# Kernel tuning notes

Hardware: AMD Instinct MI355X
Metric: run time of the kernel (lower is better)

Reference implementation:

```python
import jax, jax.numpy as jnp
import numpy as np

H = 2048      # hidden_size
K = 1024      # bottleneck_size
R = 3         # number of roles
B = 8         # batch
S = 2048      # sequence length
LN_EPS = 1e-5


def setup_inputs() -> dict:
    key = jax.random.key(0)
    ks = jax.random.split(key, 8)
    # torch nn.Linear default init ~ U(-1/sqrt(fan_in), 1/sqrt(fan_in)); scale similarly
    sd_d = 1.0 / np.sqrt(H)
    sd_u = 1.0 / np.sqrt(K)
    return {
        "role": jax.random.randint(ks[0], (B,), 0, R),
        "hidden_states": jax.random.normal(ks[1], (B, S, H), dtype=jnp.float32),
        # stacked per-role adapter params
        "W_down": jax.random.uniform(ks[2], (R, H, K), jnp.float32, -sd_d, sd_d),
        "b_down": jax.random.uniform(ks[3], (R, K), jnp.float32, -sd_d, sd_d),
        "W_up": jax.random.uniform(ks[4], (R, K, H), jnp.float32, -sd_u, sd_u),
        "b_up": jax.random.uniform(ks[5], (R, H), jnp.float32, -sd_u, sd_u),
        "gamma": jnp.ones((R, H), jnp.float32),
        "beta": jnp.zeros((R, H), jnp.float32),
    }


def reference(role, hidden_states, W_down, b_down, W_up, b_up, gamma, beta):
    # gather per-sample adapter params by role id: [B, H, K] etc.
    h = jnp.einsum("bsh,bhk->bsk", hidden_states, W_down[role]) + b_down[role][:, None, :]
    h = jax.nn.gelu(h, approximate=False)  # torch nn.GELU default = exact erf
    u = jnp.einsum("bsk,bkh->bsh", h, W_up[role]) + b_up[role][:, None, :]
    y = hidden_states + u
    # LayerNorm over last dim
    mean = jnp.mean(y, axis=-1, keepdims=True)
    var = jnp.mean(jnp.square(y - mean), axis=-1, keepdims=True)
    yn = (y - mean) * jax.lax.rsqrt(var + LN_EPS)
    return yn * gamma[role][:, None, :] + beta[role][:, None, :]
```

## Files before the change

kernel.cpp:

```cpp
#include <hip/hip_runtime.h>
#include <hip/hip_bf16.h>

#define H 2048
#define K 1024
#define R 3
#define BB 8
#define S 2048

typedef __bf16 bf16x8 __attribute__((ext_vector_type(8)));
typedef float f32x4 __attribute__((ext_vector_type(4)));
typedef unsigned short ushort8 __attribute__((ext_vector_type(8)));

static __device__ __forceinline__ unsigned short f2bf(float f) {
    unsigned int u = __float_as_uint(f);
    u += 0x7FFFu + ((u >> 16) & 1u);
    return (unsigned short)(u >> 16);
}

#define GLOAD_LDS16(g, l)                                                      \
    __builtin_amdgcn_global_load_lds(                                          \
        (const __attribute__((address_space(1))) void*)(g),                    \
        (__attribute__((address_space(3))) void*)(l), 16, 0, 0)

__global__ __launch_bounds__(256) void cvt_hs(const float* __restrict__ in,
                                              unsigned short* __restrict__ out,
                                              int n8) {
    int stride = gridDim.x * blockDim.x;
    for (int i = blockIdx.x * blockDim.x + threadIdx.x; i < n8; i += stride) {
        const float4* p = (const float4*)(in + (size_t)i * 8);
        float4 a = p[0], b = p[1];
        union { unsigned short us[8]; ushort8 v; } o;
        o.us[0] = f2bf(a.x); o.us[1] = f2bf(a.y);
        o.us[2] = f2bf(a.z); o.us[3] = f2bf(a.w);
        o.us[4] = f2bf(b.x); o.us[5] = f2bf(b.y);
        o.us[6] = f2bf(b.z); o.us[7] = f2bf(b.w);
        *(ushort8*)(out + (size_t)i * 8) = o.v;
    }
}

__global__ __launch_bounds__(256) void tpose(const float* __restrict__ in,
                                             unsigned short* __restrict__ out,
                                             int rows, int cols) {
    __shared__ float tile[32][33];
    int rr = blockIdx.z;
    const float* ip = in + (size_t)rr * rows * cols;
    unsigned short* op = out + (size_t)rr * rows * cols;
    int x = blockIdx.x * 32 + threadIdx.x;
    int y0 = blockIdx.y * 32 + threadIdx.y;
#pragma unroll
    for (int j = 0; j < 32; j += 8)
        tile[threadIdx.y + j][threadIdx.x] = ip[(size_t)(y0 + j) * cols + x];
    __syncthreads();
    int ox = blockIdx.y * 32 + threadIdx.x;
    int oy0 = blockIdx.x * 32 + threadIdx.y;
#pragma unroll
    for (int j = 0; j < 32; j += 8)
        op[(size_t)(oy0 + j) * rows + ox] = f2bf(tile[threadIdx.x][threadIdx.y + j]);
}

template <int KC, int EPI>
__global__ __launch_bounds__(512, 4) void gemm_tlp(
    const unsigned short* __restrict__ A, const unsigned short* __restrict__ Bt,
    const int* __restrict__ role, const float* __restrict__ bias,
    const unsigned short* __restrict__ resid, void* __restrict__ Out,
    float2* __restrict__ Part, int N) {
    constexpr int NT = KC / 32;
    __shared__ char smem[73728];
    const int tid = threadIdx.x;
    const int wid = tid >> 6, lane = tid & 63;
    const int wm = wid >> 2, wn = wid & 3;
    const int lr = lane & 15, lc = lane >> 4;

    const int nx = N >> 8;
    const int cpx = gridDim.x >> 3;
    const int orig = (blockIdx.x & 7) * cpx + (blockIdx.x >> 3);
    const int tn = orig % nx;
    const int tmz = orig / nx;
    const int tm = tmz & 15;
    const int z = tmz >> 4;
    const int r = role[z];

    const char* Ab = (const char*)(A + ((size_t)z * S + (size_t)tm * 128) * KC);
    const char* Bb = (const char*)(Bt + ((size_t)r * N + (size_t)tn * 256) * KC);

    const int P16 = tid * 16;
    const int srowA = P16 >> 6;
    const int sslot = ((P16 >> 4) & 3) ^ ((srowA >> 1) & 3);
    const size_t sgA = (size_t)srowA * (KC * 2) + sslot * 16;

#define STGA(sb, kt) GLOAD_LDS16(Ab + sgA + (kt) * 64, smem + (sb) + P16)
#define STGB(sb, kt, c)                                                        \
    GLOAD_LDS16(Bb + (size_t)((c) * 128 + srowA) * (KC * 2) + sslot * 16 +     \
                    (kt) * 64,                                                 \
                smem + (sb) + 8192 + (c) * 8192 + P16)
#define STAGE3(sb, kt) do { STGA(sb, kt); STGB(sb, kt, 0); STGB(sb, kt, 1); } while (0)

    STAGE3(0, 0);
    STAGE3(24576, 1);
    asm volatile("s_waitcnt vmcnt(3)" ::: "memory");
    __builtin_amdgcn_s_barrier();

    f32x4 acc[4][4] = {};
    const int ck = (lc ^ ((lr >> 1) & 3)) << 4;
    const char* sm = smem;

    int sA = 0, sB = 24576, sC = 49152;
#pragma unroll 1
    for (int t = 0; t < NT; ++t) {
        const bool pf = (t + 2) < NT;
        if (pf) STAGE3(sC, t + 2);
        bf16x8 a[4], b[4];
#pragma unroll
        for (int i = 0; i < 4; i++)
            a[i] = *(const bf16x8*)(sm + sA + ((wm * 64 + i * 16 + lr) << 6) + ck);
#pragma unroll
        for (int j = 0; j < 4; j++)
            b[j] = *(const bf16x8*)(sm + sA + 8192 + ((wn * 64 + j * 16 + lr) << 6) + ck);
        __builtin_amdgcn_s_setprio(1);
#pragma unroll
        for (int i = 0; i < 4; i++)
#pragma unroll
            for (int j = 0; j < 4; j++)
                acc[i][j] = __builtin_amdgcn_mfma_f32_16x16x32_bf16(a[i], b[j], acc[i][j], 0, 0, 0);
        __builtin_amdgcn_s_setprio(0);
        if (t < NT - 1) {
            if (pf) asm volatile("s_waitcnt vmcnt(3)" ::: "memory");
            else    asm volatile("s_waitcnt vmcnt(0)" ::: "memory");
            __builtin_amdgcn_s_barrier();
        }
        int tmp = sA; sA = sB; sB = sC; sC = tmp;
    }
#undef STGA
#undef STGB
#undef STAGE3

    const int base_m = tm * 128 + wm * 64;
    const int base_n = tn * 256 + wn * 64;
    float bn[4];
    const float* bp = bias + (size_t)r * N + base_n;
#pragma unroll
    for (int j = 0; j < 4; j++) bn[j] = bp[j * 16 + lr];

    if (EPI == 0) {
        unsigned short* o = (unsigned short*)Out;
#pragma unroll
        for (int i = 0; i < 4; i++) {
#pragma unroll
            for (int j = 0; j < 4; j++) {
#pragma unroll
                for (int q = 0; q < 4; q++) {
                    size_t grow = (size_t)z * S + base_m + i * 16 + lc * 4 + q;
                    int col = base_n + j * 16 + lr;
                    float x = acc[i][j][q] + bn[j];
                    float g = 0.5f * x * (1.0f + erff(x * 0.70710678118654752f));
                    o[grow * N + col] = f2bf(g);
                }
            }
        }
    } else {
        unsigned short* o = (unsigned short*)Out;
        float* pl = (float*)smem;
        __syncthreads();
#pragma unroll
        for (int i = 0; i < 4; i++) {
#pragma unroll
            for (int q = 0; q < 4; q++) {
                size_t grow = (size_t)z * S + base_m + i * 16 + lc * 4 + q;
                float s = 0.f, sq = 0.f;
#pragma unroll
                for (int j = 0; j < 4; j++) {
                    int col = base_n + j * 16 + lr;
                    float rv = __uint_as_float(((unsigned)resid[grow * (size_t)N + col]) << 16);
                    float y = acc[i][j][q] + bn[j] + rv;
                    o[grow * (size_t)N + col] = f2bf(y);
                    s += y; sq += y * y;
                }
#pragma unroll
                for (int off = 1; off < 16; off <<= 1) {
                    s  += __shfl_xor(s, off);
                    sq += __shfl_xor(sq, off);
                }
                if (lr == 0) {
                    int rloc = wm * 64 + i * 16 + lc * 4 + q;
                    pl[wn * 128 + rloc] = s;
                    pl[512 + wn * 128 + rloc] = sq;
                }
            }
        }
        __syncthreads();
        if (tid < 128) {
            float s  = pl[tid] + pl[128 + tid] + pl[256 + tid] + pl[384 + tid];
            float sq = pl[512 + tid] + pl[640 + tid] + pl[768 + tid] + pl[896 + tid];
            size_t grow = (size_t)z * S + tm * 128 + tid;
            Part[(size_t)tn * (BB * S) + grow] = make_float2(s, sq);
        }
    }
}

__global__ __launch_bounds__(256) void ln2(const unsigned short* __restrict__ ybf,
                                           const float2* __restrict__ part,
                                           const int* __restrict__ role,
                                           const float* __restrict__ gamma,
                                           const float* __restrict__ beta,
                                           float* __restrict__ out) {
    int row = blockIdx.x;
    int z = row >> 11;
    int r = role[z];
    float s = 0.f, ss = 0.f;
#pragma unroll
    for (int nb = 0; nb < 8; nb++) {
        float2 p = part[(size_t)nb * (BB * S) + row];
        s += p.x; ss += p.y;
    }
    float mean = s * (1.0f / H);
    float var = ss * (1.0f / H) - mean * mean;
    float rstd = rsqrtf(var + 1e-5f);
    int t = threadIdx.x;
    ushort8 yv = ((const ushort8*)(ybf + (size_t)row * H))[t];
    const float4* gp = (const float4*)(gamma + (size_t)r * H);
    const float4* bp = (const float4*)(beta + (size_t)r * H);
    float4 g0 = gp[2 * t], g1 = gp[2 * t + 1];
    float4 b0 = bp[2 * t], b1 = bp[2 * t + 1];
    float yo[8];
#pragma unroll
    for (int e = 0; e < 8; e++)
        yo[e] = (__uint_as_float(((unsigned)yv[e]) << 16) - mean) * rstd;
    float4 r0, r1;
    r0.x = yo[0] * g0.x + b0.x; r0.y = yo[1] * g0.y + b0.y;
    r0.z = yo[2] * g0.z + b0.z; r0.w = yo[3] * g0.w + b0.w;
    r1.x = yo[4] * g1.x + b1.x; r1.y = yo[5] * g1.y + b1.y;
    r1.z = yo[6] * g1.z + b1.z; r1.w = yo[7] * g1.w + b1.w;
    float4* op = (float4*)(out + (size_t)row * H);
    op[2 * t] = r0;
    op[2 * t + 1] = r1;
}

extern "C" void kernel_launch(void* const* d_in, const int* in_sizes, int n_in,
                              void* d_out, int out_size, void* d_ws, size_t ws_size,
                              hipStream_t stream) {
    const int* role = (const int*)d_in[0];
    const float* hs = (const float*)d_in[1];
    const float* Wd = (const float*)d_in[2];
    const float* bd = (const float*)d_in[3];
    const float* Wu = (const float*)d_in[4];
    const float* bu = (const float*)d_in[5];
    const float* gamma = (const float*)d_in[6];
    const float* beta = (const float*)d_in[7];
    float* out = (float*)d_out;

    char* ws = (char*)d_ws;
    unsigned short* hs_bf = (unsigned short*)ws;
    unsigned short* y_bf = (unsigned short*)ws;
    unsigned short* wd_t = (unsigned short*)(ws + 67108864);
    float2* part = (float2*)(ws + 67108864);
    unsigned short* wu_t = (unsigned short*)(ws + 67108864 + 12582912);
    unsigned short* h_ws = (unsigned short*)(ws + 67108864 + 2 * 12582912);

    cvt_hs<<<4096, 256, 0, stream>>>(hs, hs_bf, (BB * S * H) / 8);
    dim3 tb(32, 8);
    tpose<<<dim3(K / 32, H / 32, R), tb, 0, stream>>>(Wd, wd_t, H, K);
    tpose<<<dim3(H / 32, K / 32, R), tb, 0, stream>>>(Wu, wu_t, K, H);
    gemm_tlp<H, 0><<<(K / 256) * 16 * BB, 512, 0, stream>>>(hs_bf, wd_t, role, bd,
                                                            nullptr, h_ws, nullptr, K);
    gemm_tlp<K, 1><<<(H / 256) * 16 * BB, 512, 0, stream>>>(h_ws, wu_t, role, bu,
                                                            hs_bf, y_bf, part, H);
    ln2<<<BB * S, 256, 0, stream>>>(y_bf, part, role, gamma, beta, out);
}
```

Measured before the change: 259.7 us.

## Fuse fp32-to-bf16 activation conversion into first GEMM's A-tile load

Removes the standalone hidden-state conversion kernel. The down-projection GEMM now reads fp32 activations through registers, converts them to bf16 and writes them to LDS, prefetching one stage ahead. The up-projection epilogue reads the fp32 residual directly. This saves a full 128MB read plus 64MB write of the activation tensor, but the first GEMM now reads twice as many A bytes. Those loads go through VGPRs with extra waitcnt/LDS-write overhead instead of direct global-to-LDS loads, which may hurt the pipeline. The residual is also now added in fp32 rather than from a bf16 copy.

```diff
diff --git a/kernel.cpp b/kernel.cpp
--- a/kernel.cpp
+++ b/kernel.cpp
@@ -21,22 +21,6 @@
     __builtin_amdgcn_global_load_lds(                                          \
         (const __attribute__((address_space(1))) void*)(g),                    \
         (__attribute__((address_space(3))) void*)(l), 16, 0, 0)
-
-__global__ __launch_bounds__(256) void cvt_hs(const float* __restrict__ in,
-                                              unsigned short* __restrict__ out,
-                                              int n8) {
-    int stride = gridDim.x * blockDim.x;
-    for (int i = blockIdx.x * blockDim.x + threadIdx.x; i < n8; i += stride) {
-        const float4* p = (const float4*)(in + (size_t)i * 8);
-        float4 a = p[0], b = p[1];
-        union { unsigned short us[8]; ushort8 v; } o;
-        o.us[0] = f2bf(a.x); o.us[1] = f2bf(a.y);
-        o.us[2] = f2bf(a.z); o.us[3] = f2bf(a.w);
-        o.us[4] = f2bf(b.x); o.us[5] = f2bf(b.y);
-        o.us[6] = f2bf(b.z); o.us[7] = f2bf(b.w);
-        *(ushort8*)(out + (size_t)i * 8) = o.v;
-    }
-}
 
 __global__ __launch_bounds__(256) void tpose(const float* __restrict__ in,
                                              unsigned short* __restrict__ out,
@@ -58,11 +42,11 @@
         op[(size_t)(oy0 + j) * rows + ox] = f2bf(tile[threadIdx.x][threadIdx.y + j]);
 }
 
-template <int KC, int EPI>
+template <int KC, int MODE>
 __global__ __launch_bounds__(512, 4) void gemm_tlp(
-    const unsigned short* __restrict__ A, const unsigned short* __restrict__ Bt,
+    const void* __restrict__ Ain, const unsigned short* __restrict__ Bt,
     const int* __restrict__ role, const float* __restrict__ bias,
-    const unsigned short* __restrict__ resid, void* __restrict__ Out,
+    const float* __restrict__ residf, void* __restrict__ Out,
     float2* __restrict__ Part, int N) {
     constexpr int NT = KC / 32;
     __shared__ char smem[73728];
@@ -80,24 +64,56 @@
     const int z = tmz >> 4;
     const int r = role[z];
 
-    const char* Ab = (const char*)(A + ((size_t)z * S + (size_t)tm * 128) * KC);
     const char* Bb = (const char*)(Bt + ((size_t)r * N + (size_t)tn * 256) * KC);
 
     const int P16 = tid * 16;
     const int srowA = P16 >> 6;
     const int sslot = ((P16 >> 4) & 3) ^ ((srowA >> 1) & 3);
-    const size_t sgA = (size_t)srowA * (KC * 2) + sslot * 16;
-
-#define STGA(sb, kt) GLOAD_LDS16(Ab + sgA + (kt) * 64, smem + (sb) + P16)
+
 #define STGB(sb, kt, c)                                                        \
     GLOAD_LDS16(Bb + (size_t)((c) * 128 + srowA) * (KC * 2) + sslot * 16 +     \
                     (kt) * 64,                                                 \
                 smem + (sb) + 8192 + (c) * 8192 + P16)
-#define STAGE3(sb, kt) do { STGA(sb, kt); STGB(sb, kt, 0); STGB(sb, kt, 1); } while (0)
-
-    STAGE3(0, 0);
-    STAGE3(24576, 1);
-    asm volatile("s_waitcnt vmcnt(3)" ::: "memory");
+
+    const char* Ab4 = nullptr;
+    const char* Ab2 = nullptr;
+    size_t sgAf = 0, sgA = 0;
+    if (MODE == 0) {
+        Ab4 = (const char*)((const float*)Ain + ((size_t)z * S + (size_t)tm * 128) * KC);
+        sgAf = (size_t)srowA * (KC * 4) + sslot * 32;
+    } else {
+        Ab2 = (const char*)((const unsigned short*)Ain + ((size_t)z * S + (size_t)tm * 128) * KC);
+        sgA = (size_t)srowA * (KC * 2) + sslot * 16;
+    }
+
+#define STGA_BF(sb, kt) GLOAD_LDS16(Ab2 + sgA + (kt) * 64, smem + (sb) + P16)
+#define CVT_WRITE(sb, u0, u1)                                                  \
+    do {                                                                       \
+        bf16x8 pk_;                                                            \
+        pk_[0] = (__bf16)(u0).x; pk_[1] = (__bf16)(u0).y;                      \
+        pk_[2] = (__bf16)(u0).z; pk_[3] = (__bf16)(u0).w;                      \
+        pk_[4] = (__bf16)(u1).x; pk_[5] = (__bf16)(u1).y;                      \
+        pk_[6] = (__bf16)(u1).z; pk_[7] = (__bf16)(u1).w;                      \
+        *(bf16x8*)(smem + (sb) + P16) = pk_;                                   \
+    } while (0)
+
+    float4 af0, af1;
+
+    if (MODE == 0) {
+        float4 p0 = *(const float4*)(Ab4 + sgAf);
+        float4 p1 = *(const float4*)(Ab4 + sgAf + 16);
+        CVT_WRITE(0, p0, p1);
+        STGB(0, 0, 0); STGB(0, 0, 1);
+        af0 = *(const float4*)(Ab4 + sgAf + 128);
+        af1 = *(const float4*)(Ab4 + sgAf + 144);
+        STGB(24576, 1, 0); STGB(24576, 1, 1);
+        asm volatile("s_waitcnt vmcnt(4)" ::: "memory");
+        asm volatile("s_waitcnt lgkmcnt(0)" ::: "memory");
+    } else {
+        STGA_BF(0, 0); STGB(0, 0, 0); STGB(0, 0, 1);
+        STGA_BF(24576, 1); STGB(24576, 1, 0); STGB(24576, 1, 1);
+        asm volatile("s_waitcnt vmcnt(3)" ::: "memory");
+    }
     __builtin_amdgcn_s_barrier();
 
     f32x4 acc[4][4] = {};
@@ -108,7 +124,16 @@
 #pragma unroll 1
     for (int t = 0; t < NT; ++t) {
         const bool pf = (t + 2) < NT;
-        if (pf) STAGE3(sC, t + 2);
+        if (MODE == 0) {
+            if (t + 1 < NT) CVT_WRITE(sB, af0, af1);
+            if (pf) {
+                af0 = *(const float4*)(Ab4 + sgAf + (size_t)(t + 2) * 128);
+                af1 = *(const float4*)(Ab4 + sgAf + (size_t)(t + 2) * 128 + 16);
+                STGB(sC, t + 2, 0); STGB(sC, t + 2, 1);
+            }
+        } else {
+            if (pf) { STGA_BF(sC, t + 2); STGB(sC, t + 2, 0); STGB(sC, t + 2, 1); }
+        }
         bf16x8 a[4], b[4];
 #pragma unroll
         for (int i = 0; i < 4; i++)
@@ -124,15 +149,21 @@
                 acc[i][j] = __builtin_amdgcn_mfma_f32_16x16x32_bf16(a[i], b[j], acc[i][j], 0, 0, 0);
         __builtin_amdgcn_s_setprio(0);
         if (t < NT - 1) {
-            if (pf) asm volatile("s_waitcnt vmcnt(3)" ::: "memory");
-            else    asm volatile("s_waitcnt vmcnt(0)" ::: "memory");
+            if (MODE == 0) {
+                if (pf) asm volatile("s_waitcnt vmcnt(4)" ::: "memory");
+                else    asm volatile("s_waitcnt vmcnt(0)" ::: "memory");
+                asm volatile("s_waitcnt lgkmcnt(0)" ::: "memory");
+            } else {
+                if (pf) asm volatile("s_waitcnt vmcnt(3)" ::: "memory");
+                else    asm volatile("s_waitcnt vmcnt(0)" ::: "memory");
+            }
             __builtin_amdgcn_s_barrier();
         }
         int tmp = sA; sA = sB; sB = sC; sC = tmp;
     }
-#undef STGA
 #undef STGB
-#undef STAGE3
+#undef STGA_BF
+#undef CVT_WRITE
 
     const int base_m = tm * 128 + wm * 64;
     const int base_n = tn * 256 + wn * 64;
@@ -141,7 +172,7 @@
 #pragma unroll
     for (int j = 0; j < 4; j++) bn[j] = bp[j * 16 + lr];
 
-    if (EPI == 0) {
+    if (MODE == 0) {
         unsigned short* o = (unsigned short*)Out;
 #pragma unroll
         for (int i = 0; i < 4; i++) {
@@ -170,8 +201,7 @@
 #pragma unroll
                 for (int j = 0; j < 4; j++) {
                     int col = base_n + j * 16 + lr;
-                    float rv = __uint_as_float(((unsigned)resid[grow * (size_t)N + col]) << 16);
-                    float y = acc[i][j][q] + bn[j] + rv;
+                    float y = acc[i][j][q] + bn[j] + residf[grow * (size_t)N + col];
                     o[grow * (size_t)N + col] = f2bf(y);
                     s += y; sq += y * y;
                 }
@@ -249,20 +279,18 @@
     float* out = (float*)d_out;
 
     char* ws = (char*)d_ws;
-    unsigned short* hs_bf = (unsigned short*)ws;
     unsigned short* y_bf = (unsigned short*)ws;
     unsigned short* wd_t = (unsigned short*)(ws + 67108864);
     float2* part = (float2*)(ws + 67108864);
     unsigned short* wu_t = (unsigned short*)(ws + 67108864 + 12582912);
     unsigned short* h_ws = (unsigned short*)(ws + 67108864 + 2 * 12582912);
 
-    cvt_hs<<<4096, 256, 0, stream>>>(hs, hs_bf, (BB * S * H) / 8);
     dim3 tb(32, 8);
     tpose<<<dim3(K / 32, H / 32, R), tb, 0, stream>>>(Wd, wd_t, H, K);
     tpose<<<dim3(H / 32, K / 32, R), tb, 0, stream>>>(Wu, wu_t, K, H);
-    gemm_tlp<H, 0><<<(K / 256) * 16 * BB, 512, 0, stream>>>(hs_bf, wd_t, role, bd,
+    gemm_tlp<H, 0><<<(K / 256) * 16 * BB, 512, 0, stream>>>(hs, wd_t, role, bd,
                                                             nullptr, h_ws, nullptr, K);
     gemm_tlp<K, 1><<<(H / 256) * 16 * BB, 512, 0, stream>>>(h_ws, wu_t, role, bu,
-                                                            hs_bf, y_bf, part, H);
+                                                            hs, y_bf, part, H);
     ln2<<<BB * S, 256, 0, stream>>>(y_bf, part, role, gamma, beta, out);
 }
```

Result: slower. 277.6 us (+6.9%).

## Switch GEMMs to 32x32x16 MFMA with slot-major LDS layout

Applied to the files above, without the earlier changes.

Replaces the 16x16x32 bf16 MFMA tiling (4x4 tiles per wave) with 32x32x16 MFMA (2x2 tiles per wave, 16-element accumulators). It also changes the shared-memory staging layout from XOR-swizzled rows to a k-slot-major layout, so each lane reads a contiguous 16-byte chunk per slot. The epilogues are remapped to the 32x32 accumulator register layout. The aim is fewer LDS reads and MFMA issues per k-step. The risk is LDS bank conflicts from the unswizzled layout and a wider shuffle reduction in the LayerNorm partials.

```diff
diff --git a/kernel.cpp b/kernel.cpp
--- a/kernel.cpp
+++ b/kernel.cpp
@@ -8,7 +8,7 @@
 #define S 2048
 
 typedef __bf16 bf16x8 __attribute__((ext_vector_type(8)));
-typedef float f32x4 __attribute__((ext_vector_type(4)));
+typedef float f32x16 __attribute__((ext_vector_type(16)));
 typedef unsigned short ushort8 __attribute__((ext_vector_type(8)));
 
 static __device__ __forceinline__ unsigned short f2bf(float f) {
@@ -59,7 +59,7 @@
 }
 
 template <int KC, int EPI>
-__global__ __launch_bounds__(512, 4) void gemm_tlp(
+__global__ __launch_bounds__(512, 4) void gemm_3232(
     const unsigned short* __restrict__ A, const unsigned short* __restrict__ Bt,
     const int* __restrict__ role, const float* __restrict__ bias,
     const unsigned short* __restrict__ resid, void* __restrict__ Out,
@@ -69,7 +69,7 @@
     const int tid = threadIdx.x;
     const int wid = tid >> 6, lane = tid & 63;
     const int wm = wid >> 2, wn = wid & 3;
-    const int lr = lane & 15, lc = lane >> 4;
+    const int l31 = lane & 31, hi = lane >> 5;
 
     const int nx = N >> 8;
     const int cpx = gridDim.x >> 3;
@@ -84,15 +84,17 @@
     const char* Bb = (const char*)(Bt + ((size_t)r * N + (size_t)tn * 256) * KC);
 
     const int P16 = tid * 16;
-    const int srowA = P16 >> 6;
-    const int sslot = ((P16 >> 4) & 3) ^ ((srowA >> 1) & 3);
-    const size_t sgA = (size_t)srowA * (KC * 2) + sslot * 16;
-
-#define STGA(sb, kt) GLOAD_LDS16(Ab + sgA + (kt) * 64, smem + (sb) + P16)
+    const int arow = (P16 >> 4) & 127, aslot = P16 >> 11;
+#define STGA(sb, kt)                                                           \
+    GLOAD_LDS16(Ab + (size_t)arow * (KC * 2) + (kt) * 64 + aslot * 16,         \
+                smem + (sb) + P16)
 #define STGB(sb, kt, c)                                                        \
-    GLOAD_LDS16(Bb + (size_t)((c) * 128 + srowA) * (KC * 2) + sslot * 16 +     \
-                    (kt) * 64,                                                 \
-                smem + (sb) + 8192 + (c) * 8192 + P16)
+    do {                                                                       \
+        int P_ = (c) * 8192 + P16;                                             \
+        int row_ = (P_ >> 4) & 255, sl_ = P_ >> 12;                            \
+        GLOAD_LDS16(Bb + (size_t)row_ * (KC * 2) + (kt) * 64 + sl_ * 16,       \
+                    smem + (sb) + 8192 + P_);                                  \
+    } while (0)
 #define STAGE3(sb, kt) do { STGA(sb, kt); STGB(sb, kt, 0); STGB(sb, kt, 1); } while (0)
 
     STAGE3(0, 0);
@@ -100,28 +102,34 @@
     asm volatile("s_waitcnt vmcnt(3)" ::: "memory");
     __builtin_amdgcn_s_barrier();
 
-    f32x4 acc[4][4] = {};
-    const int ck = (lc ^ ((lr >> 1) & 3)) << 4;
+    f32x16 acc[2][2] = {};
     const char* sm = smem;
+    const int arow0 = (wm * 64 + l31) * 16;
+    const int brow0 = (wn * 64 + l31) * 16;
 
     int sA = 0, sB = 24576, sC = 49152;
 #pragma unroll 1
     for (int t = 0; t < NT; ++t) {
         const bool pf = (t + 2) < NT;
         if (pf) STAGE3(sC, t + 2);
-        bf16x8 a[4], b[4];
-#pragma unroll
-        for (int i = 0; i < 4; i++)
-            a[i] = *(const bf16x8*)(sm + sA + ((wm * 64 + i * 16 + lr) << 6) + ck);
-#pragma unroll
-        for (int j = 0; j < 4; j++)
-            b[j] = *(const bf16x8*)(sm + sA + 8192 + ((wn * 64 + j * 16 + lr) << 6) + ck);
+        bf16x8 a[2][2], b[2][2];
+#pragma unroll
+        for (int ti = 0; ti < 2; ti++)
+#pragma unroll
+            for (int kk = 0; kk < 2; kk++) {
+                int slotg = kk * 2 + hi;
+                a[ti][kk] = *(const bf16x8*)(sm + sA + slotg * 2048 + arow0 + ti * 512);
+                b[ti][kk] = *(const bf16x8*)(sm + sA + 8192 + slotg * 4096 + brow0 + ti * 512);
+            }
         __builtin_amdgcn_s_setprio(1);
 #pragma unroll
-        for (int i = 0; i < 4; i++)
-#pragma unroll
-            for (int j = 0; j < 4; j++)
-                acc[i][j] = __builtin_amdgcn_mfma_f32_16x16x32_bf16(a[i], b[j], acc[i][j], 0, 0, 0);
+        for (int kk = 0; kk < 2; kk++)
+#pragma unroll
+            for (int ti = 0; ti < 2; ti++)
+#pragma unroll
+                for (int tj = 0; tj < 2; tj++)
+                    acc[ti][tj] = __builtin_amdgcn_mfma_f32_32x32x16_bf16(
+                        a[ti][kk], b[tj][kk], acc[ti][tj], 0, 0, 0);
         __builtin_amdgcn_s_setprio(0);
         if (t < NT - 1) {
             if (pf) asm volatile("s_waitcnt vmcnt(3)" ::: "memory");
@@ -136,22 +144,23 @@
 
     const int base_m = tm * 128 + wm * 64;
     const int base_n = tn * 256 + wn * 64;
-    float bn[4];
+    float bb[2];
     const float* bp = bias + (size_t)r * N + base_n;
 #pragma unroll
-    for (int j = 0; j < 4; j++) bn[j] = bp[j * 16 + lr];
+    for (int tj = 0; tj < 2; tj++) bb[tj] = bp[tj * 32 + l31];
 
     if (EPI == 0) {
         unsigned short* o = (unsigned short*)Out;
 #pragma unroll
-        for (int i = 0; i < 4; i++) {
-#pragma unroll
-            for (int j = 0; j < 4; j++) {
-#pragma unroll
-                for (int q = 0; q < 4; q++) {
-                    size_t grow = (size_t)z * S + base_m + i * 16 + lc * 4 + q;
-                    int col = base_n + j * 16 + lr;
-                    float x = acc[i][j][q] + bn[j];
+        for (int ti = 0; ti < 2; ti++) {
+#pragma unroll
+            for (int tj = 0; tj < 2; tj++) {
+#pragma unroll
+                for (int reg = 0; reg < 16; reg++) {
+                    int rl = (reg & 3) + 8 * (reg >> 2) + 4 * hi;
+                    size_t grow = (size_t)z * S + base_m + ti * 32 + rl;
+                    int col = base_n + tj * 32 + l31;
+                    float x = acc[ti][tj][reg] + bb[tj];
                     float g = 0.5f * x * (1.0f + erff(x * 0.70710678118654752f));
                     o[grow * N + col] = f2bf(g);
                 }
@@ -162,26 +171,27 @@
         float* pl = (float*)smem;
         __syncthreads();
 #pragma unroll
-        for (int i = 0; i < 4; i++) {
-#pragma unroll
-            for (int q = 0; q < 4; q++) {
-                size_t grow = (size_t)z * S + base_m + i * 16 + lc * 4 + q;
+        for (int ti = 0; ti < 2; ti++) {
+#pragma unroll
+            for (int reg = 0; reg < 16; reg++) {
+                int rl = (reg & 3) + 8 * (reg >> 2) + 4 * hi;
+                size_t grow = (size_t)z * S + base_m + ti * 32 + rl;
                 float s = 0.f, sq = 0.f;
 #pragma unroll
-                for (int j = 0; j < 4; j++) {
-                    int col = base_n + j * 16 + lr;
+                for (int tj = 0; tj < 2; tj++) {
+                    int col = base_n + tj * 32 + l31;
                     float rv = __uint_as_float(((unsigned)resid[grow * (size_t)N + col]) << 16);
-                    float y = acc[i][j][q] + bn[j] + rv;
+                    float y = acc[ti][tj][reg] + bb[tj] + rv;
                     o[grow * (size_t)N + col] = f2bf(y);
                     s += y; sq += y * y;
                 }
 #pragma unroll
-                for (int off = 1; off < 16; off <<= 1) {
+                for (int off = 1; off < 32; off <<= 1) {
                     s  += __shfl_xor(s, off);
                     sq += __shfl_xor(sq, off);
                 }
-                if (lr == 0) {
-                    int rloc = wm * 64 + i * 16 + lc * 4 + q;
+                if (l31 == 0) {
+                    int rloc = wm * 64 + ti * 32 + rl;
                     pl[wn * 128 + rloc] = s;
                     pl[512 + wn * 128 + rloc] = sq;
                 }
@@ -260,9 +270,9 @@
     dim3 tb(32, 8);
     tpose<<<dim3(K / 32, H / 32, R), tb, 0, stream>>>(Wd, wd_t, H, K);
     tpose<<<dim3(H / 32, K / 32, R), tb, 0, stream>>>(Wu, wu_t, K, H);
-    gemm_tlp<H, 0><<<(K / 256) * 16 * BB, 512, 0, stream>>>(hs_bf, wd_t, role, bd,
-                                                            nullptr, h_ws, nullptr, K);
-    gemm_tlp<K, 1><<<(H / 256) * 16 * BB, 512, 0, stream>>>(h_ws, wu_t, role, bu,
-                                                            hs_bf, y_bf, part, H);
+    gemm_3232<H, 0><<<(K / 256) * 16 * BB, 512, 0, stream>>>(hs_bf, wd_t, role, bd,
+                                                             nullptr, h_ws, nullptr, K);
+    gemm_3232<K, 1><<<(H / 256) * 16 * BB, 512, 0, stream>>>(h_ws, wu_t, role, bu,
+                                                             hs_bf, y_bf, part, H);
     ln2<<<BB * S, 256, 0, stream>>>(y_bf, part, role, gamma, beta, out);
 }
```

Result: slower. 387.3 us (+49.1%).
